# Kernel optimization log

Hardware: AMD Instinct MI355X
Metric: run time of the kernel (lower is better)

The kernel has to match this reference:

```python
import jax, jax.numpy as jnp
import numpy as np

N = 50000        # n_nodes
E = 640000       # n_edges
D = 128          # d_model (in_dim == out_dim)
H = 8            # num_heads
DH = D // H      # head dim = 16
EPS = 1e-5


def _batchnorm(x, g, b):
    # BatchNorm1d, training-mode batch statistics (biased variance)
    mu = jnp.mean(x, axis=0)
    var = jnp.mean((x - mu) ** 2, axis=0)
    return (x - mu) * jax.lax.rsqrt(var + EPS) * g + b


def setup_inputs() -> dict:
    key = jax.random.key(0)
    ks = jax.random.split(key, 16)
    s = 0.05
    h = jax.random.normal(ks[0], (N, D), jnp.float32)
    src = jax.random.randint(ks[1], (E,), 0, N)
    # guarantee every node has >= 1 incoming edge (avoids z == 0)
    dst = jnp.concatenate([jnp.arange(N), jax.random.randint(ks[2], (E - N,), 0, N)])
    return {
        "h": h,
        "src": src,
        "dst": dst,
        "WQ": jax.random.normal(ks[3], (D, D), jnp.float32) * s,
        "WK": jax.random.normal(ks[4], (D, D), jnp.float32) * s,
        "WV": jax.random.normal(ks[5], (D, D), jnp.float32) * s,
        "WO": jax.random.normal(ks[6], (D, D), jnp.float32) * s,
        "bO": jnp.zeros((D,), jnp.float32),
        "W1": jax.random.normal(ks[7], (2 * D, D), jnp.float32) * s,
        "b1": jnp.zeros((2 * D,), jnp.float32),
        "W2": jax.random.normal(ks[8], (D, 2 * D), jnp.float32) * s,
        "b2": jnp.zeros((D,), jnp.float32),
        "bn1_g": jnp.ones((D,), jnp.float32),
        "bn1_b": jnp.zeros((D,), jnp.float32),
        "bn2_g": jnp.ones((D,), jnp.float32),
        "bn2_b": jnp.zeros((D,), jnp.float32),
    }


def reference(h, src, dst, WQ, WK, WV, WO, bO, W1, b1, W2, b2, bn1_g, bn1_b, bn2_g, bn2_b):
    n = h.shape[0]
    # projections -> [N, H, DH]
    Q = (h @ WQ.T).reshape(n, H, DH)
    K = (h @ WK.T).reshape(n, H, DH)
    V = (h @ WV.T).reshape(n, H, DH)
    # per-edge score: sum(K[src] * Q[dst]) -> [E, H]; clamp/exp (scaled_exp)
    score = jnp.sum(K[src] * Q[dst], axis=-1) / np.sqrt(DH)
    score = jnp.exp(jnp.clip(score, -5.0, 5.0))
    # scatter-sum weighted values and normalizers to destination nodes
    wV = jax.ops.segment_sum(V[src] * score[..., None], dst, num_segments=n)  # [N,H,DH]
    z = jax.ops.segment_sum(score, dst, num_segments=n)                       # [N,H]
    attn = (wV / z[..., None]).reshape(n, D)
    # O projection + residual + BN1
    h1 = _batchnorm(h + (attn @ WO.T + bO), bn1_g, bn1_b)
    # FFN + residual + BN2
    f = jax.nn.relu(h1 @ W1.T + b1) @ W2.T + b2
    return _batchnorm(h1 + f, bn2_g, bn2_b)
```

## Files before the change

### kernel.cpp

```cpp
#include <hip/hip_runtime.h>
#include <math.h>


#define ND128 16384
typedef _Float16 f16;
typedef __attribute__((ext_vector_type(8))) _Float16 h8;
typedef __attribute__((ext_vector_type(4))) _Float16 h4;
typedef __attribute__((ext_vector_type(2))) _Float16 h2;
typedef __attribute__((ext_vector_type(4))) float f4;

__device__ __forceinline__ float fdot2h(h2 a, h2 b) {
#if __has_builtin(__builtin_amdgcn_fdot2)
    return __builtin_amdgcn_fdot2(a, b, 0.f, false);
#else
    return (float)a[0] * (float)b[0] + (float)a[1] * (float)b[1];
#endif
}

__device__ __forceinline__ float fast_exp2(float x) {
#if __has_builtin(__builtin_amdgcn_exp2f)
    return __builtin_amdgcn_exp2f(x);
#else
    return exp2f(x);
#endif
}

template <int CTRL>
__device__ __forceinline__ float dppadd(float x) {
    int t = __builtin_amdgcn_update_dpp(0, __float_as_int(x), CTRL, 0xF, 0xF, false);
    return x + __int_as_float(t);
}
__device__ __forceinline__ float wsum8(float p) {
    p = dppadd<0xB1>(p);
    p = dppadd<0x4E>(p);
    p = dppadd<0x141>(p);
    return p;
}

__global__ __launch_bounds__(256) void k_prep_hist(
    const float* __restrict__ h, f16* __restrict__ hb,
    const float* __restrict__ WQ, const float* __restrict__ WK,
    const float* __restrict__ WV, const float* __restrict__ WO,
    const float* __restrict__ W2,
    f16* __restrict__ Wqb, f16* __restrict__ Wkb,
    f16* __restrict__ Wvb, f16* __restrict__ Wob, f16* __restrict__ W2b,
    int* __restrict__ cursor, const int* __restrict__ dst,
    int N, int E, int nhb)
{
    const int tid = threadIdx.x;
    if (blockIdx.x < (unsigned)nhb) {
        int e = blockIdx.x * 256 + tid;
        if (e < E) atomicAdd(&cursor[dst[e]], 1);
        return;
    }
    const int p = blockIdx.x - nhb;
    const int slab = p >> 1, my = p & 1;
#pragma unroll
    for (int it2 = 0; it2 < 4; ++it2) {
        int it = my * 4 + it2;
        int cid = it * 256 + tid;
        int lane = cid & 63;
        int m = (cid >> 6) & 7;
        int kb = cid >> 9;
        int row = slab * 128 + m * 16 + (lane & 15);
        int col = kb * 32 + (lane >> 4) * 8;
        f16 o8[8];
        if (row < N) {
            const float* pp = h + (size_t)row * 128 + col;
            float4 f0 = *(const float4*)pp;
            float4 f1 = *(const float4*)(pp + 4);
            o8[0] = (f16)f0.x; o8[1] = (f16)f0.y; o8[2] = (f16)f0.z; o8[3] = (f16)f0.w;
            o8[4] = (f16)f1.x; o8[5] = (f16)f1.y; o8[6] = (f16)f1.z; o8[7] = (f16)f1.w;
        } else {
#pragma unroll
            for (int j = 0; j < 8; ++j) o8[j] = (f16)0.f;
        }
        *(h8*)(hb + (size_t)slab * ND128 + (size_t)cid * 8) = *(const h8*)o8;
    }
    if (slab < 6 && my == 1) {
        const float* Wsrc; f16* dstw; int K, base;
        if (slab < 4) {
            Wsrc = slab == 0 ? WQ : slab == 1 ? WK : slab == 2 ? WV : WO;
            dstw = slab == 0 ? Wqb : slab == 1 ? Wkb : slab == 2 ? Wvb : Wob;
            K = 128; base = 0;
        } else {
            Wsrc = W2; dstw = W2b; K = 256; base = (slab - 4) * 2048;
        }
#pragma unroll
        for (int it = 0; it < 8; ++it) {
            int cid = base + it * 256 + tid;
            int lane = cid & 63;
            int kb, nt;
            if (K == 128) { kb = (cid >> 6) & 3; nt = cid >> 8; }
            else          { kb = (cid >> 6) & 7; nt = cid >> 9; }
            int row = nt * 16 + (lane & 15);
            int col = kb * 32 + (lane >> 4) * 8;
            const float* pp = Wsrc + (size_t)row * K + col;
            f16 o8[8];
#pragma unroll
            for (int j = 0; j < 8; ++j) o8[j] = (f16)pp[j];
            *(h8*)(dstw + (size_t)cid * 8) = *(const h8*)o8;
        }
    }
}

__global__ __launch_bounds__(256) void k_qkv_scan(
    const f16* __restrict__ hb, const f16* __restrict__ Wqb,
    const f16* __restrict__ Wkb, const f16* __restrict__ Wvb,
    f16* __restrict__ Qb, f16* __restrict__ KVb,
    int* __restrict__ cursor, int* __restrict__ rowptr,
    int* __restrict__ ready, int N, int nsb)
{
    const int tid = threadIdx.x;
    if (blockIdx.x < (unsigned)nsb) {
        const int b = blockIdx.x;
        int base = b * 2048 + tid * 8;
        int loc[8];
        int s = 0;
#pragma unroll
        for (int j = 0; j < 8; ++j) {
            int idx = base + j;
            loc[j] = (idx < N) ? cursor[idx] : 0;
            s += loc[j];
        }
        __shared__ int part[256];
        part[tid] = s;
        __syncthreads();
        for (int off = 1; off < 256; off <<= 1) {
            int v = (tid >= off) ? part[tid - off] : 0;
            __syncthreads();
            part[tid] += v;
            __syncthreads();
        }
        __shared__ int sboff_sh;
        if (tid == 0) {
            int prev = 0;
            if (b > 0) {
                int r;
                while ((r = __hip_atomic_load(&ready[b - 1], __ATOMIC_ACQUIRE,
                                              __HIP_MEMORY_SCOPE_AGENT)) == 0) {}
                prev = r - 1;
            }
            int btotal = part[255];
            __hip_atomic_store(&ready[b], prev + btotal + 1, __ATOMIC_RELEASE,
                               __HIP_MEMORY_SCOPE_AGENT);
            sboff_sh = prev;
            if (b == nsb - 1) rowptr[N] = prev + btotal;
        }
        __syncthreads();
        int run = sboff_sh + (tid ? part[tid - 1] : 0);
#pragma unroll
        for (int j = 0; j < 8; ++j) {
            int idx = base + j;
            if (idx < N) { rowptr[idx] = run; cursor[idx] = run; run += loc[j]; }
        }
        return;
    }
    const int b2 = blockIdx.x - nsb;
    const int slab = b2 / 6, r6 = b2 % 6;
    const int oidx = r6 >> 1, mh = r6 & 1;
    const int w = tid >> 6, lane = tid & 63;
    const f16* __restrict__ Wb = oidx == 0 ? Wqb : oidx == 1 ? Wkb : Wvb;
    const f16* A = hb + (size_t)slab * ND128;

    h8 bfr[2][4];
#pragma unroll
    for (int nt = 0; nt < 2; ++nt)
#pragma unroll
        for (int kb = 0; kb < 4; ++kb)
            bfr[nt][kb] = *(const h8*)(Wb + (size_t)(((2 * w + nt) * 4 + kb) * 64 + lane) * 8);

    f4 acc[4][2];
    f4 zero = {0.f, 0.f, 0.f, 0.f};
#pragma unroll
    for (int m = 0; m < 4; ++m) { acc[m][0] = zero; acc[m][1] = zero; }

#pragma unroll
    for (int m = 0; m < 4; ++m) {
        int mg = mh * 4 + m;
#pragma unroll
        for (int kb = 0; kb < 4; ++kb) {
            h8 a = *(const h8*)(A + (size_t)((kb * 8 + mg) * 64 + lane) * 8);
            acc[m][0] = __builtin_amdgcn_mfma_f32_16x16x32_f16(bfr[0][kb], a, acc[m][0], 0, 0, 0);
            acc[m][1] = __builtin_amdgcn_mfma_f32_16x16x32_f16(bfr[1][kb], a, acc[m][1], 0, 0, 0);
        }
    }

    const int rl = lane & 15, quad = lane >> 4;
#pragma unroll
    for (int m = 0; m < 4; ++m) {
        int gr = slab * 128 + (mh * 4 + m) * 16 + rl;
        if (gr < N) {
#pragma unroll
            for (int nt = 0; nt < 2; ++nt) {
                h4 o;
                o[0] = (f16)acc[m][nt][0]; o[1] = (f16)acc[m][nt][1];
                o[2] = (f16)acc[m][nt][2]; o[3] = (f16)acc[m][nt][3];
                int col = w * 32 + nt * 16 + quad * 4;
                if (oidx == 0) {
                    *(h4*)(Qb + (size_t)gr * 128 + col) = o;
                } else {
                    *(h4*)(KVb + (size_t)gr * 256 + (oidx == 1 ? col : 128 + col)) = o;
                }
            }
        }
    }
}

__global__ __launch_bounds__(256) void k_scatter(
    const int* __restrict__ src, const int* __restrict__ dst,
    int* __restrict__ cursor, int* __restrict__ csr_src, int E)
{
    int e = blockIdx.x * 256 + threadIdx.x;
    if (e < E) {
        int pos = atomicAdd(&cursor[dst[e]], 1);
        csr_src[pos] = src[e];
    }
}

__global__ __launch_bounds__(256) void k_attn(
    const f16* __restrict__ Qb, const f16* __restrict__ KVb,
    const int* __restrict__ rowptr, const int* __restrict__ csr_src,
    f16* __restrict__ attnf, int N)
{
    const int node = blockIdx.x * 4 + (threadIdx.x >> 6);
    const int lane = threadIdx.x & 63;
    if (node >= N) return;
    const int beg = rowptr[node], end = rowptr[node + 1];

    h2 qs;
    {
        h2 q2 = ((const h2*)(Qb + (size_t)node * 128))[lane];
        const float SCL = 0.25f * 1.44269504f;
        qs[0] = (f16)((float)q2[0] * SCL);
        qs[1] = (f16)((float)q2[1] * SCL);
    }
    const float CLP = 5.f * 1.44269504f;

    const h2* __restrict__ KV2 = (const h2*)KVb;

    h2 accA, accB;
    accA[0] = (f16)0.f; accA[1] = (f16)0.f;
    accB[0] = (f16)0.f; accB[1] = (f16)0.f;
    float z = 0.f;

    int i = beg;
    for (; i + 7 < end; i += 8) {
        int s[8];
#pragma unroll
        for (int u = 0; u < 8; ++u) s[u] = csr_src[i + u];
        h2 kk[8], vv[8];
#pragma unroll
        for (int u = 0; u < 8; ++u) {
            const h2* row = KV2 + (size_t)s[u] * 128;
            kk[u] = row[lane];
            vv[u] = row[64 + lane];
        }
        float sc[8];
#pragma unroll
        for (int u = 0; u < 8; ++u) {
            float p = wsum8(fdot2h(qs, kk[u]));
            sc[u] = fast_exp2(fminf(fmaxf(p, -CLP), CLP));
        }
#pragma unroll
        for (int u = 0; u < 8; ++u) z += sc[u];
#pragma unroll
        for (int u = 0; u < 8; ++u) {
            h2 c; c[0] = (f16)sc[u]; c[1] = (f16)sc[u];
            if (u & 1) accB += c * vv[u]; else accA += c * vv[u];
        }
    }
    if (i + 3 < end) {
        int s[4];
#pragma unroll
        for (int u = 0; u < 4; ++u) s[u] = csr_src[i + u];
        h2 kk[4], vv[4];
#pragma unroll
        for (int u = 0; u < 4; ++u) {
            const h2* row = KV2 + (size_t)s[u] * 128;
            kk[u] = row[lane];
            vv[u] = row[64 + lane];
        }
#pragma unroll
        for (int u = 0; u < 4; ++u) {
            float p = wsum8(fdot2h(qs, kk[u]));
            float scu = fast_exp2(fminf(fmaxf(p, -CLP), CLP));
            z += scu;
            h2 c; c[0] = (f16)scu; c[1] = (f16)scu;
            if (u & 1) accB += c * vv[u]; else accA += c * vv[u];
        }
        i += 4;
    }
    for (; i < end; ++i) {
        int s0 = csr_src[i];
        const h2* row = KV2 + (size_t)s0 * 128;
        h2 k0 = row[lane];
        h2 v0 = row[64 + lane];
        float p0 = wsum8(fdot2h(qs, k0));
        float sc0 = fast_exp2(fminf(fmaxf(p0, -CLP), CLP));
        z += sc0;
        h2 c0; c0[0] = (f16)sc0; c0[1] = (f16)sc0;
        accA += c0 * v0;
    }

    float inv = 1.f / z;
    float ax = ((float)accA[0] + (float)accB[0]) * inv;
    float ay = ((float)accA[1] + (float)accB[1]) * inv;
    h2 o2;
    o2[0] = (f16)ax; o2[1] = (f16)ay;
    int slab = node >> 7, m = (node >> 4) & 7, lr = node & 15;
    int kb = lane >> 4, quad2 = (lane & 15) >> 2, j = (lane & 3) * 2;
    *(h2*)(attnf + (size_t)slab * ND128 +
           (size_t)(((kb * 8 + m) * 64 + lr + 16 * quad2) * 8 + j)) = o2;
}

__global__ __launch_bounds__(256) void k_oproj(
    const f16* __restrict__ attnf, const f16* __restrict__ Wob,
    const float* __restrict__ h, const float* __restrict__ bO,
    f16* __restrict__ t1b, float* __restrict__ bn, int N)
{
    __shared__ float csum[128], csq[128];
    const int tid = threadIdx.x, slab = blockIdx.x, mh = blockIdx.y;
    const int w = tid >> 6, lane = tid & 63;
    if (tid < 128) { csum[tid] = 0.f; csq[tid] = 0.f; }
    __syncthreads();
    const f16* A = attnf + (size_t)slab * ND128;

    h8 bfr[2][4];
#pragma unroll
    for (int nt = 0; nt < 2; ++nt)
#pragma unroll
        for (int kb = 0; kb < 4; ++kb)
            bfr[nt][kb] = *(const h8*)(Wob + (size_t)(((2 * w + nt) * 4 + kb) * 64 + lane) * 8);

    f4 acc[4][2];
    f4 zero = {0.f, 0.f, 0.f, 0.f};
#pragma unroll
    for (int m = 0; m < 4; ++m) { acc[m][0] = zero; acc[m][1] = zero; }
#pragma unroll
    for (int m = 0; m < 4; ++m) {
        int mg = mh * 4 + m;
#pragma unroll
        for (int kb = 0; kb < 4; ++kb) {
            h8 a = *(const h8*)(A + (size_t)((kb * 8 + mg) * 64 + lane) * 8);
            acc[m][0] = __builtin_amdgcn_mfma_f32_16x16x32_f16(bfr[0][kb], a, acc[m][0], 0, 0, 0);
            acc[m][1] = __builtin_amdgcn_mfma_f32_16x16x32_f16(bfr[1][kb], a, acc[m][1], 0, 0, 0);
        }
    }

    const int rl = lane & 15, quad = lane >> 4;
    float4 bo[2];
#pragma unroll
    for (int nt = 0; nt < 2; ++nt)
        bo[nt] = *(const float4*)(bO + w * 32 + nt * 16 + quad * 4);
    float pcs[2][4], pcq[2][4];
#pragma unroll
    for (int nt = 0; nt < 2; ++nt)
#pragma unroll
        for (int r = 0; r < 4; ++r) { pcs[nt][r] = 0.f; pcq[nt][r] = 0.f; }

#pragma unroll
    for (int m = 0; m < 4; ++m) {
        int mg = mh * 4 + m;
        int gr = slab * 128 + mg * 16 + rl;
        if (gr < N) {
#pragma unroll
            for (int nt = 0; nt < 2; ++nt) {
                int col0 = w * 32 + nt * 16 + quad * 4;
                float4 hv = *(const float4*)(h + (size_t)gr * 128 + col0);
                float v0 = acc[m][nt][0] + hv.x + bo[nt].x;
                float v1 = acc[m][nt][1] + hv.y + bo[nt].y;
                float v2 = acc[m][nt][2] + hv.z + bo[nt].z;
                float v3 = acc[m][nt][3] + hv.w + bo[nt].w;
                h4 o; o[0] = (f16)v0; o[1] = (f16)v1; o[2] = (f16)v2; o[3] = (f16)v3;
                *(h4*)(t1b + (size_t)slab * ND128 +
                       (size_t)(((w * 8 + mg) * 64 + (nt * 2 + (quad >> 1)) * 16 + rl) * 8 +
                                (quad & 1) * 4)) = o;
                pcs[nt][0] += v0; pcq[nt][0] += v0 * v0;
                pcs[nt][1] += v1; pcq[nt][1] += v1 * v1;
                pcs[nt][2] += v2; pcq[nt][2] += v2 * v2;
                pcs[nt][3] += v3; pcq[nt][3] += v3 * v3;
            }
        }
    }
#pragma unroll
    for (int nt = 0; nt < 2; ++nt)
#pragma unroll
        for (int r = 0; r < 4; ++r) {
            float s = pcs[nt][r], q = pcq[nt][r];
            s += __shfl_xor(s, 8, 16); q += __shfl_xor(q, 8, 16);
            s += __shfl_xor(s, 4, 16); q += __shfl_xor(q, 4, 16);
            s += __shfl_xor(s, 2, 16); q += __shfl_xor(q, 2, 16);
            s += __shfl_xor(s, 1, 16); q += __shfl_xor(q, 1, 16);
            if (rl == 0) {
                int cl = w * 32 + nt * 16 + quad * 4 + r;
                atomicAdd(&csum[cl], s);
                atomicAdd(&csq[cl], q);
            }
        }
    __syncthreads();
    if (tid < 128) {
        atomicAdd(bn + tid, csum[tid]);
        atomicAdd(bn + 128 + tid, csq[tid]);
    }
}

__global__ __launch_bounds__(128) void k_fold1(
    const float* __restrict__ bn, const float* __restrict__ g1,
    const float* __restrict__ bb1, const float* __restrict__ W1,
    const float* __restrict__ b1, f16* __restrict__ W1b,
    float* __restrict__ badj, float* __restrict__ sfold,
    float* __restrict__ bfold, int N)
{
    const int o = blockIdx.x, i = threadIdx.x;
    float invN = 1.f / (float)N;
    float mu = bn[i] * invN;
    float var = bn[128 + i] * invN - mu * mu;
    float s = g1[i] * rsqrtf(var + 1e-5f);
    float bb = bb1[i] - mu * s;
    if (o == 0) { sfold[i] = s; bfold[i] = bb; }
    float wv = W1[(size_t)o * 128 + i];
    __shared__ float red[128];
    red[i] = wv * bb;
    const int nt = o >> 4, lanelow = o & 15;
    const int kb = i >> 5, quad = (i >> 3) & 3, j = i & 7;
    W1b[(size_t)(((nt * 4 + kb) * 64 + lanelow + 16 * quad) * 8 + j)] = (f16)(wv * s);
    __syncthreads();
#pragma unroll
    for (int off = 64; off; off >>= 1) {
        if (i < off) red[i] += red[i + off];
        __syncthreads();
    }
    if (i == 0) badj[o] = b1[o] + red[0];
}

__global__ __launch_bounds__(256) void k_ffn1(
    const f16* __restrict__ t1b, const f16* __restrict__ W1b,
    const float* __restrict__ badj, f16* __restrict__ ub, int N)
{
    const int slab = blockIdx.x, ch = blockIdx.y, mh = blockIdx.z;
    const int w = threadIdx.x >> 6, lane = threadIdx.x & 63;
    const f16* A = t1b + (size_t)slab * ND128;

    h8 bfr[2][4];
#pragma unroll
    for (int nt = 0; nt < 2; ++nt)
#pragma unroll
        for (int kb = 0; kb < 4; ++kb) {
            int ntg = ch * 8 + 2 * w + nt;
            bfr[nt][kb] = *(const h8*)(W1b + (size_t)((ntg * 4 + kb) * 64 + lane) * 8);
        }

    f4 acc[4][2];
    f4 zero = {0.f, 0.f, 0.f, 0.f};
#pragma unroll
    for (int m = 0; m < 4; ++m) { acc[m][0] = zero; acc[m][1] = zero; }
#pragma unroll
    for (int m = 0; m < 4; ++m) {
        int mg = mh * 4 + m;
#pragma unroll
        for (int kb = 0; kb < 4; ++kb) {
            h8 a = *(const h8*)(A + (size_t)((kb * 8 + mg) * 64 + lane) * 8);
            acc[m][0] = __builtin_amdgcn_mfma_f32_16x16x32_f16(bfr[0][kb], a, acc[m][0], 0, 0, 0);
            acc[m][1] = __builtin_amdgcn_mfma_f32_16x16x32_f16(bfr[1][kb], a, acc[m][1], 0, 0, 0);
        }
    }

    const int rl = lane & 15, quad = lane >> 4;
    const int kbu = ch * 4 + w;
    float4 ba[2];
#pragma unroll
    for (int nt = 0; nt < 2; ++nt)
        ba[nt] = *(const float4*)(badj + ch * 128 + w * 32 + nt * 16 + quad * 4);
#pragma unroll
    for (int m = 0; m < 4; ++m) {
        int mg = mh * 4 + m;
        int gr = slab * 128 + mg * 16 + rl;
        if (gr < N) {
#pragma unroll
            for (int nt = 0; nt < 2; ++nt) {
                h4 o;
                o[0] = (f16)fmaxf(acc[m][nt][0] + ba[nt].x, 0.f);
                o[1] = (f16)fmaxf(acc[m][nt][1] + ba[nt].y, 0.f);
                o[2] = (f16)fmaxf(acc[m][nt][2] + ba[nt].z, 0.f);
                o[3] = (f16)fmaxf(acc[m][nt][3] + ba[nt].w, 0.f);
                *(h4*)(ub + (size_t)slab * 32768 +
                       (size_t)(((kbu * 8 + mg) * 64 + (nt * 2 + (quad >> 1)) * 16 + rl) * 8 +
                                (quad & 1) * 4)) = o;
            }
        }
    }
}

__global__ __launch_bounds__(256) void k_ffn2(
    const f16* __restrict__ ub, const f16* __restrict__ W2b,
    const f16* __restrict__ t1b,
    const float* __restrict__ sfold, const float* __restrict__ bfold,
    const float* __restrict__ b2, float* __restrict__ out,
    float* __restrict__ bn, int N)
{
    __shared__ float csum[128], csq[128], sS[128], sB[128];
    const int tid = threadIdx.x, slab = blockIdx.x, mh = blockIdx.y;
    const int w = tid >> 6, lane = tid & 63;
    if (tid < 128) {
        csum[tid] = 0.f; csq[tid] = 0.f;
        sS[tid] = sfold[tid]; sB[tid] = bfold[tid] + b2[tid];
    }
    __syncthreads();
    const f16* A = ub + (size_t)slab * 32768;
    const f16* T1 = t1b + (size_t)slab * ND128;

    h8 bfr[2][8];
#pragma unroll
    for (int nt = 0; nt < 2; ++nt)
#pragma unroll
        for (int kb = 0; kb < 8; ++kb)
            bfr[nt][kb] = *(const h8*)(W2b + (size_t)(((2 * w + nt) * 8 + kb) * 64 + lane) * 8);

    f4 acc[4][2];
    f4 zero = {0.f, 0.f, 0.f, 0.f};
#pragma unroll
    for (int m = 0; m < 4; ++m) { acc[m][0] = zero; acc[m][1] = zero; }
#pragma unroll
    for (int m = 0; m < 4; ++m) {
        int mg = mh * 4 + m;
#pragma unroll
        for (int kb = 0; kb < 8; ++kb) {
            h8 a = *(const h8*)(A + (size_t)((kb * 8 + mg) * 64 + lane) * 8);
            acc[m][0] = __builtin_amdgcn_mfma_f32_16x16x32_f16(bfr[0][kb], a, acc[m][0], 0, 0, 0);
            acc[m][1] = __builtin_amdgcn_mfma_f32_16x16x32_f16(bfr[1][kb], a, acc[m][1], 0, 0, 0);
        }
    }

    const int rl = lane & 15, quad = lane >> 4;
    float pcs[2][4], pcq[2][4];
#pragma unroll
    for (int nt = 0; nt < 2; ++nt)
#pragma unroll
        for (int r = 0; r < 4; ++r) { pcs[nt][r] = 0.f; pcq[nt][r] = 0.f; }

#pragma unroll
    for (int m = 0; m < 4; ++m) {
        int mg = mh * 4 + m;
        int gr = slab * 128 + mg * 16 + rl;
        if (gr < N) {
#pragma unroll
            for (int nt = 0; nt < 2; ++nt) {
                int col0 = w * 32 + nt * 16 + quad * 4;
                h4 t1v = *(const h4*)(T1 +
                    (size_t)(((w * 8 + mg) * 64 + (nt * 2 + (quad >> 1)) * 16 + rl) * 8 +
                             (quad & 1) * 4));
                float4 ss = *(const float4*)&sS[col0];
                float4 sb = *(const float4*)&sB[col0];
                float4 o;
                o.x = acc[m][nt][0] + fmaf(ss.x, (float)t1v[0], sb.x);
                o.y = acc[m][nt][1] + fmaf(ss.y, (float)t1v[1], sb.y);
                o.z = acc[m][nt][2] + fmaf(ss.z, (float)t1v[2], sb.z);
                o.w = acc[m][nt][3] + fmaf(ss.w, (float)t1v[3], sb.w);
                *(float4*)(out + (size_t)gr * 128 + col0) = o;
                pcs[nt][0] += o.x; pcq[nt][0] += o.x * o.x;
                pcs[nt][1] += o.y; pcq[nt][1] += o.y * o.y;
                pcs[nt][2] += o.z; pcq[nt][2] += o.z * o.z;
                pcs[nt][3] += o.w; pcq[nt][3] += o.w * o.w;
            }
        }
    }
#pragma unroll
    for (int nt = 0; nt < 2; ++nt)
#pragma unroll
        for (int r = 0; r < 4; ++r) {
            float s = pcs[nt][r], q = pcq[nt][r];
            s += __shfl_xor(s, 8, 16); q += __shfl_xor(q, 8, 16);
            s += __shfl_xor(s, 4, 16); q += __shfl_xor(q, 4, 16);
            s += __shfl_xor(s, 2, 16); q += __shfl_xor(q, 2, 16);
            s += __shfl_xor(s, 1, 16); q += __shfl_xor(q, 1, 16);
            if (rl == 0) {
                int cl = w * 32 + nt * 16 + quad * 4 + r;
                atomicAdd(&csum[cl], s);
                atomicAdd(&csq[cl], q);
            }
        }
    __syncthreads();
    if (tid < 128) {
        atomicAdd(bn + 256 + tid, csum[tid]);
        atomicAdd(bn + 384 + tid, csq[tid]);
    }
}

__global__ __launch_bounds__(256) void k_bn2(
    float* __restrict__ out, const float* __restrict__ bn,
    const float* __restrict__ g2, const float* __restrict__ bb2, int N)
{
    __shared__ float sS[128], sB[128];
    const int tid = threadIdx.x;
    if (tid < 128) {
        float invN = 1.f / (float)N;
        float mu = bn[256 + tid] * invN;
        float var = bn[384 + tid] * invN - mu * mu;
        float scl = g2[tid] * rsqrtf(var + 1e-5f);
        sS[tid] = scl;
        sB[tid] = bb2[tid] - mu * scl;
    }
    __syncthreads();
    size_t idx = (size_t)blockIdx.x * 256 + tid;
    size_t total = (size_t)N * 32;
    if (idx < total) {
        int c0 = (int)((idx * 4) & 127);
        float4 v = *(const float4*)(out + idx * 4);
        v.x = fmaf(v.x, sS[c0 + 0], sB[c0 + 0]);
        v.y = fmaf(v.y, sS[c0 + 1], sB[c0 + 1]);
        v.z = fmaf(v.z, sS[c0 + 2], sB[c0 + 2]);
        v.w = fmaf(v.w, sS[c0 + 3], sB[c0 + 3]);
        *(float4*)(out + idx * 4) = v;
    }
}

extern "C" void kernel_launch(void* const* d_in, const int* in_sizes, int n_in,
                              void* d_out, int out_size, void* d_ws, size_t ws_size,
                              hipStream_t stream)
{
    const float* h   = (const float*)d_in[0];
    const int*   src = (const int*)d_in[1];
    const int*   dst = (const int*)d_in[2];
    const float* WQ  = (const float*)d_in[3];
    const float* WK  = (const float*)d_in[4];
    const float* WV  = (const float*)d_in[5];
    const float* WO  = (const float*)d_in[6];
    const float* bO  = (const float*)d_in[7];
    const float* W1  = (const float*)d_in[8];
    const float* b1  = (const float*)d_in[9];
    const float* W2  = (const float*)d_in[10];
    const float* b2  = (const float*)d_in[11];
    const float* g1  = (const float*)d_in[12];
    const float* bb1 = (const float*)d_in[13];
    const float* g2  = (const float*)d_in[14];
    const float* bb2 = (const float*)d_in[15];
    float* out = (float*)d_out;

    int N = in_sizes[0] / 128;
    int E = in_sizes[1];
    const int slabs = (N + 127) / 128;
    const int nsb = (N + 2047) / 2048;
    const int nhb = (E + 255) / 256;
    const size_t B1 = (size_t)slabs * 32768;

    char* Wp = (char*)d_ws;
    f16* hb  = (f16*)Wp;
    f16* Qb  = (f16*)(Wp + B1);
    f16* KVb = (f16*)(Wp + 2 * B1);
    f16* ub  = (f16*)(Wp + B1);
    f16* t1b = (f16*)(Wp + 3 * B1);
    const size_t base = 4 * B1;
    f16* Wqb = (f16*)(Wp + base);
    f16* Wkb = (f16*)(Wp + base + 32768);
    f16* Wvb = (f16*)(Wp + base + 65536);
    f16* Wob = (f16*)(Wp + base + 98304);
    f16* W1b = (f16*)(Wp + base + 131072);
    f16* W2b = (f16*)(Wp + base + 196608);
    float* badj  = (float*)(Wp + base + 262144);
    float* sfold = (float*)(Wp + base + 263168);
    float* bfold = (float*)(Wp + base + 263680);
    float* bn    = (float*)(Wp + base + 264192);
    int* ready   = (int*)(Wp + base + 266240);
    int* cursor  = (int*)(Wp + base + 266496);
    int* rowptr  = (int*)(Wp + base + 266496 + (size_t)N * 4);
    int* csr     = (int*)(Wp + base + 266496 + (size_t)N * 8 + 8);

    hipMemsetAsync(Wp + base + 264192, 0, 2304 + (size_t)N * 4, stream);
    k_prep_hist<<<nhb + slabs * 2, 256, 0, stream>>>(
        h, hb, WQ, WK, WV, WO, W2, Wqb, Wkb, Wvb, Wob, W2b, cursor, dst, N, E, nhb);
    k_qkv_scan<<<nsb + slabs * 6, 256, 0, stream>>>(
        hb, Wqb, Wkb, Wvb, Qb, KVb, cursor, rowptr, ready, N, nsb);
    k_scatter<<<nhb, 256, 0, stream>>>(src, dst, cursor, csr, E);
    k_attn<<<(N + 3) / 4, 256, 0, stream>>>(Qb, KVb, rowptr, csr, hb, N);
    k_oproj<<<dim3(slabs, 2), 256, 0, stream>>>(hb, Wob, h, bO, t1b, bn, N);
    k_fold1<<<256, 128, 0, stream>>>(bn, g1, bb1, W1, b1, W1b, badj, sfold, bfold, N);
    k_ffn1<<<dim3(slabs, 2, 2), 256, 0, stream>>>(t1b, W1b, badj, ub, N);
    k_ffn2<<<dim3(slabs, 2), 256, 0, stream>>>(ub, W2b, t1b, sfold, bfold, b2, out, bn, N);
    k_bn2<<<(int)(((size_t)N * 32 + 255) / 256), 256, 0, stream>>>(out, bn, g2, bb2, N);
}
```

Baseline: 340.1 us.

## Fuse front and back stages into persistent cooperative kernels with grid syncs

Merges the memset, fp16 conversion, histogram, QKV projection and prefix scan into one cooperative kernel, and merges O-projection, BN1 fold, FFN1, FFN2 and the BN2 apply into another. Stages are separated by grid.sync, and each block loops over work units with a grid stride. The chained decoupled scan is replaced by a two-pass block-sum scan. This removes several kernel launches and the memset, at the cost of grid-wide barriers, a grid sized to occupancy, and less parallelism in stages that had many blocks.

```diff
diff --git a/kernel.cpp b/kernel.cpp
--- a/kernel.cpp
+++ b/kernel.cpp
@@ -1,5 +1,8 @@
 #include <hip/hip_runtime.h>
+#include <hip/hip_cooperative_groups.h>
 #include <math.h>
+
+namespace cg = cooperative_groups;
 
 
 #define ND128 16384
@@ -37,81 +40,156 @@
     return p;
 }
 
-__global__ __launch_bounds__(256) void k_prep_hist(
+__global__ __launch_bounds__(256) void k_front(
     const float* __restrict__ h, f16* __restrict__ hb,
     const float* __restrict__ WQ, const float* __restrict__ WK,
     const float* __restrict__ WV, const float* __restrict__ WO,
     const float* __restrict__ W2,
     f16* __restrict__ Wqb, f16* __restrict__ Wkb,
     f16* __restrict__ Wvb, f16* __restrict__ Wob, f16* __restrict__ W2b,
-    int* __restrict__ cursor, const int* __restrict__ dst,
-    int N, int E, int nhb)
-{
-    const int tid = threadIdx.x;
-    if (blockIdx.x < (unsigned)nhb) {
-        int e = blockIdx.x * 256 + tid;
-        if (e < E) atomicAdd(&cursor[dst[e]], 1);
-        return;
-    }
-    const int p = blockIdx.x - nhb;
-    const int slab = p >> 1, my = p & 1;
-#pragma unroll
-    for (int it2 = 0; it2 < 4; ++it2) {
-        int it = my * 4 + it2;
-        int cid = it * 256 + tid;
-        int lane = cid & 63;
-        int m = (cid >> 6) & 7;
-        int kb = cid >> 9;
-        int row = slab * 128 + m * 16 + (lane & 15);
-        int col = kb * 32 + (lane >> 4) * 8;
-        f16 o8[8];
-        if (row < N) {
-            const float* pp = h + (size_t)row * 128 + col;
-            float4 f0 = *(const float4*)pp;
-            float4 f1 = *(const float4*)(pp + 4);
-            o8[0] = (f16)f0.x; o8[1] = (f16)f0.y; o8[2] = (f16)f0.z; o8[3] = (f16)f0.w;
-            o8[4] = (f16)f1.x; o8[5] = (f16)f1.y; o8[6] = (f16)f1.z; o8[7] = (f16)f1.w;
-        } else {
-#pragma unroll
-            for (int j = 0; j < 8; ++j) o8[j] = (f16)0.f;
-        }
-        *(h8*)(hb + (size_t)slab * ND128 + (size_t)cid * 8) = *(const h8*)o8;
-    }
-    if (slab < 6 && my == 1) {
-        const float* Wsrc; f16* dstw; int K, base;
-        if (slab < 4) {
-            Wsrc = slab == 0 ? WQ : slab == 1 ? WK : slab == 2 ? WV : WO;
-            dstw = slab == 0 ? Wqb : slab == 1 ? Wkb : slab == 2 ? Wvb : Wob;
-            K = 128; base = 0;
-        } else {
-            Wsrc = W2; dstw = W2b; K = 256; base = (slab - 4) * 2048;
-        }
-#pragma unroll
-        for (int it = 0; it < 8; ++it) {
-            int cid = base + it * 256 + tid;
-            int lane = cid & 63;
-            int kb, nt;
-            if (K == 128) { kb = (cid >> 6) & 3; nt = cid >> 8; }
-            else          { kb = (cid >> 6) & 7; nt = cid >> 9; }
-            int row = nt * 16 + (lane & 15);
-            int col = kb * 32 + (lane >> 4) * 8;
-            const float* pp = Wsrc + (size_t)row * K + col;
-            f16 o8[8];
-#pragma unroll
-            for (int j = 0; j < 8; ++j) o8[j] = (f16)pp[j];
-            *(h8*)(dstw + (size_t)cid * 8) = *(const h8*)o8;
-        }
-    }
-}
-
-__global__ __launch_bounds__(256) void k_qkv_scan(
-    const f16* __restrict__ hb, const f16* __restrict__ Wqb,
-    const f16* __restrict__ Wkb, const f16* __restrict__ Wvb,
     f16* __restrict__ Qb, f16* __restrict__ KVb,
     int* __restrict__ cursor, int* __restrict__ rowptr,
-    int* __restrict__ ready, int N, int nsb)
+    int* __restrict__ bsum, float* __restrict__ bn,
+    const int* __restrict__ dst, int N, int E, int nhb, int nsb, int slabs)
 {
+    cg::grid_group grid = cg::this_grid();
     const int tid = threadIdx.x;
+    const int G = gridDim.x;
+    __shared__ int part[256];
+    __shared__ int sboff_sh;
+
+    for (int idx = blockIdx.x * 256 + tid; idx < N; idx += G * 256) cursor[idx] = 0;
+    if (blockIdx.x == 0) { bn[tid] = 0.f; bn[tid + 256] = 0.f; }
+    const int U0 = slabs * 2 + 6;
+    for (int u = blockIdx.x; u < U0; u += G) {
+        if (u < slabs * 2) {
+            const int slab = u >> 1, my = u & 1;
+#pragma unroll
+            for (int it2 = 0; it2 < 4; ++it2) {
+                int it = my * 4 + it2;
+                int cid = it * 256 + tid;
+                int lane = cid & 63;
+                int m = (cid >> 6) & 7;
+                int kb = cid >> 9;
+                int row = slab * 128 + m * 16 + (lane & 15);
+                int col = kb * 32 + (lane >> 4) * 8;
+                f16 o8[8];
+                if (row < N) {
+                    const float* pp = h + (size_t)row * 128 + col;
+                    float4 f0 = *(const float4*)pp;
+                    float4 f1 = *(const float4*)(pp + 4);
+                    o8[0] = (f16)f0.x; o8[1] = (f16)f0.y; o8[2] = (f16)f0.z; o8[3] = (f16)f0.w;
+                    o8[4] = (f16)f1.x; o8[5] = (f16)f1.y; o8[6] = (f16)f1.z; o8[7] = (f16)f1.w;
+                } else {
+#pragma unroll
+                    for (int j = 0; j < 8; ++j) o8[j] = (f16)0.f;
+                }
+                *(h8*)(hb + (size_t)slab * ND128 + (size_t)cid * 8) = *(const h8*)o8;
+            }
+        } else {
+            const int ws = u - slabs * 2;
+            const float* Wsrc; f16* dstw; int K, base;
+            if (ws < 4) {
+                Wsrc = ws == 0 ? WQ : ws == 1 ? WK : ws == 2 ? WV : WO;
+                dstw = ws == 0 ? Wqb : ws == 1 ? Wkb : ws == 2 ? Wvb : Wob;
+                K = 128; base = 0;
+            } else {
+                Wsrc = W2; dstw = W2b; K = 256; base = (ws - 4) * 2048;
+            }
+#pragma unroll
+            for (int it = 0; it < 8; ++it) {
+                int cid = base + it * 256 + tid;
+                int lane = cid & 63;
+                int kb, nt;
+                if (K == 128) { kb = (cid >> 6) & 3; nt = cid >> 8; }
+                else          { kb = (cid >> 6) & 7; nt = cid >> 9; }
+                int row = nt * 16 + (lane & 15);
+                int col = kb * 32 + (lane >> 4) * 8;
+                const float* pp = Wsrc + (size_t)row * K + col;
+                f16 o8[8];
+#pragma unroll
+                for (int j = 0; j < 8; ++j) o8[j] = (f16)pp[j];
+                *(h8*)(dstw + (size_t)cid * 8) = *(const h8*)o8;
+            }
+        }
+    }
+    grid.sync();
+
+    const int U1 = nhb + slabs * 6;
+    for (int u = blockIdx.x; u < U1; u += G) {
+        if (u < nhb) {
+            int e = u * 256 + tid;
+            if (e < E) atomicAdd(&cursor[dst[e]], 1);
+        } else {
+            const int b2 = u - nhb;
+            const int slab = b2 / 6, r6 = b2 % 6;
+            const int oidx = r6 >> 1, mh = r6 & 1;
+            const int w = tid >> 6, lane = tid & 63;
+            const f16* __restrict__ Wb = oidx == 0 ? Wqb : oidx == 1 ? Wkb : Wvb;
+            const f16* A = hb + (size_t)slab * ND128;
+
+            h8 bfr[2][4];
+#pragma unroll
+            for (int nt = 0; nt < 2; ++nt)
+#pragma unroll
+                for (int kb = 0; kb < 4; ++kb)
+                    bfr[nt][kb] = *(const h8*)(Wb + (size_t)(((2 * w + nt) * 4 + kb) * 64 + lane) * 8);
+
+            f4 acc[4][2];
+            f4 zero = {0.f, 0.f, 0.f, 0.f};
+#pragma unroll
+            for (int m = 0; m < 4; ++m) { acc[m][0] = zero; acc[m][1] = zero; }
+#pragma unroll
+            for (int m = 0; m < 4; ++m) {
+                int mg = mh * 4 + m;
+#pragma unroll
+                for (int kb = 0; kb < 4; ++kb) {
+                    h8 a = *(const h8*)(A + (size_t)((kb * 8 + mg) * 64 + lane) * 8);
+                    acc[m][0] = __builtin_amdgcn_mfma_f32_16x16x32_f16(bfr[0][kb], a, acc[m][0], 0, 0, 0);
+                    acc[m][1] = __builtin_amdgcn_mfma_f32_16x16x32_f16(bfr[1][kb], a, acc[m][1], 0, 0, 0);
+                }
+            }
+            const int rl = lane & 15, quad = lane >> 4;
+#pragma unroll
+            for (int m = 0; m < 4; ++m) {
+                int gr = slab * 128 + (mh * 4 + m) * 16 + rl;
+                if (gr < N) {
+#pragma unroll
+                    for (int nt = 0; nt < 2; ++nt) {
+                        h4 o;
+                        o[0] = (f16)acc[m][nt][0]; o[1] = (f16)acc[m][nt][1];
+                        o[2] = (f16)acc[m][nt][2]; o[3] = (f16)acc[m][nt][3];
+                        int col = w * 32 + nt * 16 + quad * 4;
+                        if (oidx == 0) {
+                            *(h4*)(Qb + (size_t)gr * 128 + col) = o;
+                        } else {
+                            *(h4*)(KVb + (size_t)gr * 256 + (oidx == 1 ? col : 128 + col)) = o;
+                        }
+                    }
+                }
+            }
+        }
+    }
+    grid.sync();
+
+    if (blockIdx.x < (unsigned)nsb) {
+        int base = blockIdx.x * 2048 + tid * 8;
+        int s = 0;
+#pragma unroll
+        for (int j = 0; j < 8; ++j) {
+            int idx = base + j;
+            if (idx < N) s += cursor[idx];
+        }
+        part[tid] = s;
+        __syncthreads();
+        for (int off = 128; off; off >>= 1) {
+            if (tid < off) part[tid] += part[tid + off];
+            __syncthreads();
+        }
+        if (tid == 0) bsum[blockIdx.x] = part[0];
+    }
+    grid.sync();
+
     if (blockIdx.x < (unsigned)nsb) {
         const int b = blockIdx.x;
         int base = b * 2048 + tid * 8;
@@ -123,7 +201,6 @@
             loc[j] = (idx < N) ? cursor[idx] : 0;
             s += loc[j];
         }
-        __shared__ int part[256];
         part[tid] = s;
         __syncthreads();
         for (int off = 1; off < 256; off <<= 1) {
@@ -132,20 +209,11 @@
             part[tid] += v;
             __syncthreads();
         }
-        __shared__ int sboff_sh;
         if (tid == 0) {
             int prev = 0;
-            if (b > 0) {
-                int r;
-                while ((r = __hip_atomic_load(&ready[b - 1], __ATOMIC_ACQUIRE,
-                                              __HIP_MEMORY_SCOPE_AGENT)) == 0) {}
-                prev = r - 1;
-            }
-            int btotal = part[255];
-            __hip_atomic_store(&ready[b], prev + btotal + 1, __ATOMIC_RELEASE,
-                               __HIP_MEMORY_SCOPE_AGENT);
+            for (int i2 = 0; i2 < b; ++i2) prev += bsum[i2];
             sboff_sh = prev;
-            if (b == nsb - 1) rowptr[N] = prev + btotal;
+            if (b == nsb - 1) rowptr[N] = prev + part[255];
         }
         __syncthreads();
         int run = sboff_sh + (tid ? part[tid - 1] : 0);
@@ -153,56 +221,6 @@
         for (int j = 0; j < 8; ++j) {
             int idx = base + j;
             if (idx < N) { rowptr[idx] = run; cursor[idx] = run; run += loc[j]; }
-        }
-        return;
-    }
-    const int b2 = blockIdx.x - nsb;
-    const int slab = b2 / 6, r6 = b2 % 6;
-    const int oidx = r6 >> 1, mh = r6 & 1;
-    const int w = tid >> 6, lane = tid & 63;
-    const f16* __restrict__ Wb = oidx == 0 ? Wqb : oidx == 1 ? Wkb : Wvb;
-    const f16* A = hb + (size_t)slab * ND128;
-
-    h8 bfr[2][4];
-#pragma unroll
-    for (int nt = 0; nt < 2; ++nt)
-#pragma unroll
-        for (int kb = 0; kb < 4; ++kb)
-            bfr[nt][kb] = *(const h8*)(Wb + (size_t)(((2 * w + nt) * 4 + kb) * 64 + lane) * 8);
-
-    f4 acc[4][2];
-    f4 zero = {0.f, 0.f, 0.f, 0.f};
-#pragma unroll
-    for (int m = 0; m < 4; ++m) { acc[m][0] = zero; acc[m][1] = zero; }
-
-#pragma unroll
-    for (int m = 0; m < 4; ++m) {
-        int mg = mh * 4 + m;
-#pragma unroll
-        for (int kb = 0; kb < 4; ++kb) {
-            h8 a = *(const h8*)(A + (size_t)((kb * 8 + mg) * 64 + lane) * 8);
-            acc[m][0] = __builtin_amdgcn_mfma_f32_16x16x32_f16(bfr[0][kb], a, acc[m][0], 0, 0, 0);
-            acc[m][1] = __builtin_amdgcn_mfma_f32_16x16x32_f16(bfr[1][kb], a, acc[m][1], 0, 0, 0);
-        }
-    }
-
-    const int rl = lane & 15, quad = lane >> 4;
-#pragma unroll
-    for (int m = 0; m < 4; ++m) {
-        int gr = slab * 128 + (mh * 4 + m) * 16 + rl;
-        if (gr < N) {
-#pragma unroll
-            for (int nt = 0; nt < 2; ++nt) {
-                h4 o;
-                o[0] = (f16)acc[m][nt][0]; o[1] = (f16)acc[m][nt][1];
-                o[2] = (f16)acc[m][nt][2]; o[3] = (f16)acc[m][nt][3];
-                int col = w * 32 + nt * 16 + quad * 4;
-                if (oidx == 0) {
-                    *(h4*)(Qb + (size_t)gr * 128 + col) = o;
-                } else {
-                    *(h4*)(KVb + (size_t)gr * 256 + (oidx == 1 ? col : 128 + col)) = o;
-                }
-            }
         }
     }
 }
@@ -314,285 +332,278 @@
            (size_t)(((kb * 8 + m) * 64 + lr + 16 * quad2) * 8 + j)) = o2;
 }
 
-__global__ __launch_bounds__(256) void k_oproj(
+__global__ __launch_bounds__(256) void k_back(
     const f16* __restrict__ attnf, const f16* __restrict__ Wob,
     const float* __restrict__ h, const float* __restrict__ bO,
-    f16* __restrict__ t1b, float* __restrict__ bn, int N)
+    f16* __restrict__ t1b, float* __restrict__ bn,
+    const float* __restrict__ g1, const float* __restrict__ bb1,
+    const float* __restrict__ W1, const float* __restrict__ b1,
+    f16* __restrict__ W1b, float* __restrict__ badj,
+    float* __restrict__ sfold, float* __restrict__ bfold,
+    f16* __restrict__ ub, const f16* __restrict__ W2b,
+    const float* __restrict__ b2, float* __restrict__ out,
+    const float* __restrict__ g2, const float* __restrict__ bb2,
+    int N, int slabs)
 {
-    __shared__ float csum[128], csq[128];
-    const int tid = threadIdx.x, slab = blockIdx.x, mh = blockIdx.y;
+    cg::grid_group grid = cg::this_grid();
+    const int tid = threadIdx.x;
+    const int G = gridDim.x;
     const int w = tid >> 6, lane = tid & 63;
-    if (tid < 128) { csum[tid] = 0.f; csq[tid] = 0.f; }
-    __syncthreads();
-    const f16* A = attnf + (size_t)slab * ND128;
-
-    h8 bfr[2][4];
-#pragma unroll
-    for (int nt = 0; nt < 2; ++nt)
-#pragma unroll
-        for (int kb = 0; kb < 4; ++kb)
-            bfr[nt][kb] = *(const h8*)(Wob + (size_t)(((2 * w + nt) * 4 + kb) * 64 + lane) * 8);
-
-    f4 acc[4][2];
-    f4 zero = {0.f, 0.f, 0.f, 0.f};
-#pragma unroll
-    for (int m = 0; m < 4; ++m) { acc[m][0] = zero; acc[m][1] = zero; }
-#pragma unroll
-    for (int m = 0; m < 4; ++m) {
-        int mg = mh * 4 + m;
-#pragma unroll
-        for (int kb = 0; kb < 4; ++kb) {
-            h8 a = *(const h8*)(A + (size_t)((kb * 8 + mg) * 64 + lane) * 8);
-            acc[m][0] = __builtin_amdgcn_mfma_f32_16x16x32_f16(bfr[0][kb], a, acc[m][0], 0, 0, 0);
-            acc[m][1] = __builtin_amdgcn_mfma_f32_16x16x32_f16(bfr[1][kb], a, acc[m][1], 0, 0, 0);
-        }
-    }
-
     const int rl = lane & 15, quad = lane >> 4;
-    float4 bo[2];
-#pragma unroll
-    for (int nt = 0; nt < 2; ++nt)
-        bo[nt] = *(const float4*)(bO + w * 32 + nt * 16 + quad * 4);
-    float pcs[2][4], pcq[2][4];
-#pragma unroll
-    for (int nt = 0; nt < 2; ++nt)
-#pragma unroll
-        for (int r = 0; r < 4; ++r) { pcs[nt][r] = 0.f; pcq[nt][r] = 0.f; }
-
-#pragma unroll
-    for (int m = 0; m < 4; ++m) {
-        int mg = mh * 4 + m;
-        int gr = slab * 128 + mg * 16 + rl;
-        if (gr < N) {
-#pragma unroll
-            for (int nt = 0; nt < 2; ++nt) {
-                int col0 = w * 32 + nt * 16 + quad * 4;
-                float4 hv = *(const float4*)(h + (size_t)gr * 128 + col0);
-                float v0 = acc[m][nt][0] + hv.x + bo[nt].x;
-                float v1 = acc[m][nt][1] + hv.y + bo[nt].y;
-                float v2 = acc[m][nt][2] + hv.z + bo[nt].z;
-                float v3 = acc[m][nt][3] + hv.w + bo[nt].w;
-                h4 o; o[0] = (f16)v0; o[1] = (f16)v1; o[2] = (f16)v2; o[3] = (f16)v3;
-                *(h4*)(t1b + (size_t)slab * ND128 +
-                       (size_t)(((w * 8 + mg) * 64 + (nt * 2 + (quad >> 1)) * 16 + rl) * 8 +
-                                (quad & 1) * 4)) = o;
-                pcs[nt][0] += v0; pcq[nt][0] += v0 * v0;
-                pcs[nt][1] += v1; pcq[nt][1] += v1 * v1;
-                pcs[nt][2] += v2; pcq[nt][2] += v2 * v2;
-                pcs[nt][3] += v3; pcq[nt][3] += v3 * v3;
-            }
-        }
-    }
-#pragma unroll
-    for (int nt = 0; nt < 2; ++nt)
-#pragma unroll
-        for (int r = 0; r < 4; ++r) {
-            float s = pcs[nt][r], q = pcq[nt][r];
-            s += __shfl_xor(s, 8, 16); q += __shfl_xor(q, 8, 16);
-            s += __shfl_xor(s, 4, 16); q += __shfl_xor(q, 4, 16);
-            s += __shfl_xor(s, 2, 16); q += __shfl_xor(q, 2, 16);
-            s += __shfl_xor(s, 1, 16); q += __shfl_xor(q, 1, 16);
-            if (rl == 0) {
-                int cl = w * 32 + nt * 16 + quad * 4 + r;
-                atomicAdd(&csum[cl], s);
-                atomicAdd(&csq[cl], q);
-            }
-        }
-    __syncthreads();
-    if (tid < 128) {
-        atomicAdd(bn + tid, csum[tid]);
-        atomicAdd(bn + 128 + tid, csq[tid]);
-    }
-}
-
-__global__ __launch_bounds__(128) void k_fold1(
-    const float* __restrict__ bn, const float* __restrict__ g1,
-    const float* __restrict__ bb1, const float* __restrict__ W1,
-    const float* __restrict__ b1, f16* __restrict__ W1b,
-    float* __restrict__ badj, float* __restrict__ sfold,
-    float* __restrict__ bfold, int N)
-{
-    const int o = blockIdx.x, i = threadIdx.x;
-    float invN = 1.f / (float)N;
-    float mu = bn[i] * invN;
-    float var = bn[128 + i] * invN - mu * mu;
-    float s = g1[i] * rsqrtf(var + 1e-5f);
-    float bb = bb1[i] - mu * s;
-    if (o == 0) { sfold[i] = s; bfold[i] = bb; }
-    float wv = W1[(size_t)o * 128 + i];
+    __shared__ float csum[128], csq[128], sS[128], sB[128];
     __shared__ float red[128];
-    red[i] = wv * bb;
-    const int nt = o >> 4, lanelow = o & 15;
-    const int kb = i >> 5, quad = (i >> 3) & 3, j = i & 7;
-    W1b[(size_t)(((nt * 4 + kb) * 64 + lanelow + 16 * quad) * 8 + j)] = (f16)(wv * s);
-    __syncthreads();
-#pragma unroll
-    for (int off = 64; off; off >>= 1) {
-        if (i < off) red[i] += red[i + off];
+
+    {
+        h8 bfr[2][4];
+#pragma unroll
+        for (int nt = 0; nt < 2; ++nt)
+#pragma unroll
+            for (int kb = 0; kb < 4; ++kb)
+                bfr[nt][kb] = *(const h8*)(Wob + (size_t)(((2 * w + nt) * 4 + kb) * 64 + lane) * 8);
+        float4 bo[2];
+#pragma unroll
+        for (int nt = 0; nt < 2; ++nt)
+            bo[nt] = *(const float4*)(bO + w * 32 + nt * 16 + quad * 4);
+
+        for (int u = blockIdx.x; u < slabs * 2; u += G) {
+            const int slab = u >> 1, mh = u & 1;
+            if (tid < 128) { csum[tid] = 0.f; csq[tid] = 0.f; }
+            __syncthreads();
+            const f16* A = attnf + (size_t)slab * ND128;
+
+            f4 acc[4][2];
+            f4 zero = {0.f, 0.f, 0.f, 0.f};
+#pragma unroll
+            for (int m = 0; m < 4; ++m) { acc[m][0] = zero; acc[m][1] = zero; }
+#pragma unroll
+            for (int m = 0; m < 4; ++m) {
+                int mg = mh * 4 + m;
+#pragma unroll
+                for (int kb = 0; kb < 4; ++kb) {
+                    h8 a = *(const h8*)(A + (size_t)((kb * 8 + mg) * 64 + lane) * 8);
+                    acc[m][0] = __builtin_amdgcn_mfma_f32_16x16x32_f16(bfr[0][kb], a, acc[m][0], 0, 0, 0);
+                    acc[m][1] = __builtin_amdgcn_mfma_f32_16x16x32_f16(bfr[1][kb], a, acc[m][1], 0, 0, 0);
+                }
+            }
+            float pcs[2][4], pcq[2][4];
+#pragma unroll
+            for (int nt = 0; nt < 2; ++nt)
+#pragma unroll
+                for (int r = 0; r < 4; ++r) { pcs[nt][r] = 0.f; pcq[nt][r] = 0.f; }
+#pragma unroll
+            for (int m = 0; m < 4; ++m) {
+                int mg = mh * 4 + m;
+                int gr = slab * 128 + mg * 16 + rl;
+                if (gr < N) {
+#pragma unroll
+                    for (int nt = 0; nt < 2; ++nt) {
+                        int col0 = w * 32 + nt * 16 + quad * 4;
+                        float4 hv = *(const float4*)(h + (size_t)gr * 128 + col0);
+                        float v0 = acc[m][nt][0] + hv.x + bo[nt].x;
+                        float v1 = acc[m][nt][1] + hv.y + bo[nt].y;
+                        float v2 = acc[m][nt][2] + hv.z + bo[nt].z;
+                        float v3 = acc[m][nt][3] + hv.w + bo[nt].w;
+                        h4 o; o[0] = (f16)v0; o[1] = (f16)v1; o[2] = (f16)v2; o[3] = (f16)v3;
+                        *(h4*)(t1b + (size_t)slab * ND128 +
+                               (size_t)(((w * 8 + mg) * 64 + (nt * 2 + (quad >> 1)) * 16 + rl) * 8 +
+                                        (quad & 1) * 4)) = o;
+                        pcs[nt][0] += v0; pcq[nt][0] += v0 * v0;
+                        pcs[nt][1] += v1; pcq[nt][1] += v1 * v1;
+                        pcs[nt][2] += v2; pcq[nt][2] += v2 * v2;
+                        pcs[nt][3] += v3; pcq[nt][3] += v3 * v3;
+                    }
+                }
+            }
+#pragma unroll
+            for (int nt = 0; nt < 2; ++nt)
+#pragma unroll
+                for (int r = 0; r < 4; ++r) {
+                    float s = pcs[nt][r], q = pcq[nt][r];
+                    s += __shfl_xor(s, 8, 16); q += __shfl_xor(q, 8, 16);
+                    s += __shfl_xor(s, 4, 16); q += __shfl_xor(q, 4, 16);
+                    s += __shfl_xor(s, 2, 16); q += __shfl_xor(q, 2, 16);
+                    s += __shfl_xor(s, 1, 16); q += __shfl_xor(q, 1, 16);
+                    if (rl == 0) {
+                        int cl = w * 32 + nt * 16 + quad * 4 + r;
+                        atomicAdd(&csum[cl], s);
+                        atomicAdd(&csq[cl], q);
+                    }
+                }
+            __syncthreads();
+            if (tid < 128) {
+                atomicAdd(bn + tid, csum[tid]);
+                atomicAdd(bn + 128 + tid, csq[tid]);
+            }
+            __syncthreads();
+        }
+    }
+    grid.sync();
+
+    for (int u = blockIdx.x; u < 256; u += G) {
+        const int o = u, i = tid & 127;
+        if (tid < 128) {
+            float invN = 1.f / (float)N;
+            float mu = bn[i] * invN;
+            float var = bn[128 + i] * invN - mu * mu;
+            float s = g1[i] * rsqrtf(var + 1e-5f);
+            float bb = bb1[i] - mu * s;
+            if (o == 0) { sfold[i] = s; bfold[i] = bb; }
+            float wv = W1[(size_t)o * 128 + i];
+            red[i] = wv * bb;
+            const int nt = o >> 4, lanelow = o & 15;
+            const int kb = i >> 5, qq = (i >> 3) & 3, j = i & 7;
+            W1b[(size_t)(((nt * 4 + kb) * 64 + lanelow + 16 * qq) * 8 + j)] = (f16)(wv * s);
+        }
         __syncthreads();
-    }
-    if (i == 0) badj[o] = b1[o] + red[0];
-}
-
-__global__ __launch_bounds__(256) void k_ffn1(
-    const f16* __restrict__ t1b, const f16* __restrict__ W1b,
-    const float* __restrict__ badj, f16* __restrict__ ub, int N)
-{
-    const int slab = blockIdx.x, ch = blockIdx.y, mh = blockIdx.z;
-    const int w = threadIdx.x >> 6, lane = threadIdx.x & 63;
-    const f16* A = t1b + (size_t)slab * ND128;
-
-    h8 bfr[2][4];
-#pragma unroll
-    for (int nt = 0; nt < 2; ++nt)
-#pragma unroll
-        for (int kb = 0; kb < 4; ++kb) {
-            int ntg = ch * 8 + 2 * w + nt;
-            bfr[nt][kb] = *(const h8*)(W1b + (size_t)((ntg * 4 + kb) * 64 + lane) * 8);
-        }
-
-    f4 acc[4][2];
-    f4 zero = {0.f, 0.f, 0.f, 0.f};
-#pragma unroll
-    for (int m = 0; m < 4; ++m) { acc[m][0] = zero; acc[m][1] = zero; }
-#pragma unroll
-    for (int m = 0; m < 4; ++m) {
-        int mg = mh * 4 + m;
-#pragma unroll
-        for (int kb = 0; kb < 4; ++kb) {
-            h8 a = *(const h8*)(A + (size_t)((kb * 8 + mg) * 64 + lane) * 8);
-            acc[m][0] = __builtin_amdgcn_mfma_f32_16x16x32_f16(bfr[0][kb], a, acc[m][0], 0, 0, 0);
-            acc[m][1] = __builtin_amdgcn_mfma_f32_16x16x32_f16(bfr[1][kb], a, acc[m][1], 0, 0, 0);
-        }
-    }
-
-    const int rl = lane & 15, quad = lane >> 4;
-    const int kbu = ch * 4 + w;
-    float4 ba[2];
-#pragma unroll
-    for (int nt = 0; nt < 2; ++nt)
-        ba[nt] = *(const float4*)(badj + ch * 128 + w * 32 + nt * 16 + quad * 4);
-#pragma unroll
-    for (int m = 0; m < 4; ++m) {
-        int mg = mh * 4 + m;
-        int gr = slab * 128 + mg * 16 + rl;
-        if (gr < N) {
-#pragma unroll
-            for (int nt = 0; nt < 2; ++nt) {
-                h4 o;
-                o[0] = (f16)fmaxf(acc[m][nt][0] + ba[nt].x, 0.f);
-                o[1] = (f16)fmaxf(acc[m][nt][1] + ba[nt].y, 0.f);
-                o[2] = (f16)fmaxf(acc[m][nt][2] + ba[nt].z, 0.f);
-                o[3] = (f16)fmaxf(acc[m][nt][3] + ba[nt].w, 0.f);
-                *(h4*)(ub + (size_t)slab * 32768 +
-                       (size_t)(((kbu * 8 + mg) * 64 + (nt * 2 + (quad >> 1)) * 16 + rl) * 8 +
-                                (quad & 1) * 4)) = o;
-            }
-        }
-    }
-}
-
-__global__ __launch_bounds__(256) void k_ffn2(
-    const f16* __restrict__ ub, const f16* __restrict__ W2b,
-    const f16* __restrict__ t1b,
-    const float* __restrict__ sfold, const float* __restrict__ bfold,
-    const float* __restrict__ b2, float* __restrict__ out,
-    float* __restrict__ bn, int N)
-{
-    __shared__ float csum[128], csq[128], sS[128], sB[128];
-    const int tid = threadIdx.x, slab = blockIdx.x, mh = blockIdx.y;
-    const int w = tid >> 6, lane = tid & 63;
-    if (tid < 128) {
-        csum[tid] = 0.f; csq[tid] = 0.f;
-        sS[tid] = sfold[tid]; sB[tid] = bfold[tid] + b2[tid];
-    }
-    __syncthreads();
-    const f16* A = ub + (size_t)slab * 32768;
-    const f16* T1 = t1b + (size_t)slab * ND128;
-
-    h8 bfr[2][8];
-#pragma unroll
-    for (int nt = 0; nt < 2; ++nt)
-#pragma unroll
-        for (int kb = 0; kb < 8; ++kb)
-            bfr[nt][kb] = *(const h8*)(W2b + (size_t)(((2 * w + nt) * 8 + kb) * 64 + lane) * 8);
-
-    f4 acc[4][2];
-    f4 zero = {0.f, 0.f, 0.f, 0.f};
-#pragma unroll
-    for (int m = 0; m < 4; ++m) { acc[m][0] = zero; acc[m][1] = zero; }
-#pragma unroll
-    for (int m = 0; m < 4; ++m) {
-        int mg = mh * 4 + m;
-#pragma unroll
-        for (int kb = 0; kb < 8; ++kb) {
-            h8 a = *(const h8*)(A + (size_t)((kb * 8 + mg) * 64 + lane) * 8);
-            acc[m][0] = __builtin_amdgcn_mfma_f32_16x16x32_f16(bfr[0][kb], a, acc[m][0], 0, 0, 0);
-            acc[m][1] = __builtin_amdgcn_mfma_f32_16x16x32_f16(bfr[1][kb], a, acc[m][1], 0, 0, 0);
-        }
-    }
-
-    const int rl = lane & 15, quad = lane >> 4;
-    float pcs[2][4], pcq[2][4];
-#pragma unroll
-    for (int nt = 0; nt < 2; ++nt)
-#pragma unroll
-        for (int r = 0; r < 4; ++r) { pcs[nt][r] = 0.f; pcq[nt][r] = 0.f; }
-
-#pragma unroll
-    for (int m = 0; m < 4; ++m) {
-        int mg = mh * 4 + m;
-        int gr = slab * 128 + mg * 16 + rl;
-        if (gr < N) {
-#pragma unroll
-            for (int nt = 0; nt < 2; ++nt) {
-                int col0 = w * 32 + nt * 16 + quad * 4;
-                h4 t1v = *(const h4*)(T1 +
-                    (size_t)(((w * 8 + mg) * 64 + (nt * 2 + (quad >> 1)) * 16 + rl) * 8 +
-                             (quad & 1) * 4));
-                float4 ss = *(const float4*)&sS[col0];
-                float4 sb = *(const float4*)&sB[col0];
-                float4 o;
-                o.x = acc[m][nt][0] + fmaf(ss.x, (float)t1v[0], sb.x);
-                o.y = acc[m][nt][1] + fmaf(ss.y, (float)t1v[1], sb.y);
-                o.z = acc[m][nt][2] + fmaf(ss.z, (float)t1v[2], sb.z);
-                o.w = acc[m][nt][3] + fmaf(ss.w, (float)t1v[3], sb.w);
-                *(float4*)(out + (size_t)gr * 128 + col0) = o;
-                pcs[nt][0] += o.x; pcq[nt][0] += o.x * o.x;
-                pcs[nt][1] += o.y; pcq[nt][1] += o.y * o.y;
-                pcs[nt][2] += o.z; pcq[nt][2] += o.z * o.z;
-                pcs[nt][3] += o.w; pcq[nt][3] += o.w * o.w;
-            }
-        }
-    }
-#pragma unroll
-    for (int nt = 0; nt < 2; ++nt)
-#pragma unroll
-        for (int r = 0; r < 4; ++r) {
-            float s = pcs[nt][r], q = pcq[nt][r];
-            s += __shfl_xor(s, 8, 16); q += __shfl_xor(q, 8, 16);
-            s += __shfl_xor(s, 4, 16); q += __shfl_xor(q, 4, 16);
-            s += __shfl_xor(s, 2, 16); q += __shfl_xor(q, 2, 16);
-            s += __shfl_xor(s, 1, 16); q += __shfl_xor(q, 1, 16);
-            if (rl == 0) {
-                int cl = w * 32 + nt * 16 + quad * 4 + r;
-                atomicAdd(&csum[cl], s);
-                atomicAdd(&csq[cl], q);
-            }
-        }
-    __syncthreads();
-    if (tid < 128) {
-        atomicAdd(bn + 256 + tid, csum[tid]);
-        atomicAdd(bn + 384 + tid, csq[tid]);
-    }
-}
-
-__global__ __launch_bounds__(256) void k_bn2(
-    float* __restrict__ out, const float* __restrict__ bn,
-    const float* __restrict__ g2, const float* __restrict__ bb2, int N)
-{
-    __shared__ float sS[128], sB[128];
-    const int tid = threadIdx.x;
+        for (int off = 64; off; off >>= 1) {
+            if (tid < off) red[tid] += red[tid + off];
+            __syncthreads();
+        }
+        if (tid == 0) badj[o] = b1[o] + red[0];
+        __syncthreads();
+    }
+    grid.sync();
+
+    for (int u = blockIdx.x; u < slabs * 4; u += G) {
+        const int slab = u >> 2, ch = (u >> 1) & 1, mh = u & 1;
+        const f16* A = t1b + (size_t)slab * ND128;
+
+        h8 bfr[2][4];
+#pragma unroll
+        for (int nt = 0; nt < 2; ++nt)
+#pragma unroll
+            for (int kb = 0; kb < 4; ++kb) {
+                int ntg = ch * 8 + 2 * w + nt;
+                bfr[nt][kb] = *(const h8*)(W1b + (size_t)((ntg * 4 + kb) * 64 + lane) * 8);
+            }
+
+        f4 acc[4][2];
+        f4 zero = {0.f, 0.f, 0.f, 0.f};
+#pragma unroll
+        for (int m = 0; m < 4; ++m) { acc[m][0] = zero; acc[m][1] = zero; }
+#pragma unroll
+        for (int m = 0; m < 4; ++m) {
+            int mg = mh * 4 + m;
+#pragma unroll
+            for (int kb = 0; kb < 4; ++kb) {
+                h8 a = *(const h8*)(A + (size_t)((kb * 8 + mg) * 64 + lane) * 8);
+                acc[m][0] = __builtin_amdgcn_mfma_f32_16x16x32_f16(bfr[0][kb], a, acc[m][0], 0, 0, 0);
+                acc[m][1] = __builtin_amdgcn_mfma_f32_16x16x32_f16(bfr[1][kb], a, acc[m][1], 0, 0, 0);
+            }
+        }
+        const int kbu = ch * 4 + w;
+        float4 ba[2];
+#pragma unroll
+        for (int nt = 0; nt < 2; ++nt)
+            ba[nt] = *(const float4*)(badj + ch * 128 + w * 32 + nt * 16 + quad * 4);
+#pragma unroll
+        for (int m = 0; m < 4; ++m) {
+            int mg = mh * 4 + m;
+            int gr = slab * 128 + mg * 16 + rl;
+            if (gr < N) {
+#pragma unroll
+                for (int nt = 0; nt < 2; ++nt) {
+                    h4 o;
+                    o[0] = (f16)fmaxf(acc[m][nt][0] + ba[nt].x, 0.f);
+                    o[1] = (f16)fmaxf(acc[m][nt][1] + ba[nt].y, 0.f);
+                    o[2] = (f16)fmaxf(acc[m][nt][2] + ba[nt].z, 0.f);
+                    o[3] = (f16)fmaxf(acc[m][nt][3] + ba[nt].w, 0.f);
+                    *(h4*)(ub + (size_t)slab * 32768 +
+                           (size_t)(((kbu * 8 + mg) * 64 + (nt * 2 + (quad >> 1)) * 16 + rl) * 8 +
+                                    (quad & 1) * 4)) = o;
+                }
+            }
+        }
+    }
+    grid.sync();
+
+    {
+        h8 bfr[2][8];
+#pragma unroll
+        for (int nt = 0; nt < 2; ++nt)
+#pragma unroll
+            for (int kb = 0; kb < 8; ++kb)
+                bfr[nt][kb] = *(const h8*)(W2b + (size_t)(((2 * w + nt) * 8 + kb) * 64 + lane) * 8);
+        if (tid < 128) { sS[tid] = sfold[tid]; sB[tid] = bfold[tid] + b2[tid]; }
+        __syncthreads();
+
+        for (int u = blockIdx.x; u < slabs * 2; u += G) {
+            const int slab = u >> 1, mh = u & 1;
+            if (tid < 128) { csum[tid] = 0.f; csq[tid] = 0.f; }
+            __syncthreads();
+            const f16* A = ub + (size_t)slab * 32768;
+            const f16* T1 = t1b + (size_t)slab * ND128;
+
+            f4 acc[4][2];
+            f4 zero = {0.f, 0.f, 0.f, 0.f};
+#pragma unroll
+            for (int m = 0; m < 4; ++m) { acc[m][0] = zero; acc[m][1] = zero; }
+#pragma unroll
+            for (int m = 0; m < 4; ++m) {
+                int mg = mh * 4 + m;
+#pragma unroll
+                for (int kb = 0; kb < 8; ++kb) {
+                    h8 a = *(const h8*)(A + (size_t)((kb * 8 + mg) * 64 + lane) * 8);
+                    acc[m][0] = __builtin_amdgcn_mfma_f32_16x16x32_f16(bfr[0][kb], a, acc[m][0], 0, 0, 0);
+                    acc[m][1] = __builtin_amdgcn_mfma_f32_16x16x32_f16(bfr[1][kb], a, acc[m][1], 0, 0, 0);
+                }
+            }
+            float pcs[2][4], pcq[2][4];
+#pragma unroll
+            for (int nt = 0; nt < 2; ++nt)
+#pragma unroll
+                for (int r = 0; r < 4; ++r) { pcs[nt][r] = 0.f; pcq[nt][r] = 0.f; }
+#pragma unroll
+            for (int m = 0; m < 4; ++m) {
+                int mg = mh * 4 + m;
+                int gr = slab * 128 + mg * 16 + rl;
+                if (gr < N) {
+#pragma unroll
+                    for (int nt = 0; nt < 2; ++nt) {
+                        int col0 = w * 32 + nt * 16 + quad * 4;
+                        h4 t1v = *(const h4*)(T1 +
+                            (size_t)(((w * 8 + mg) * 64 + (nt * 2 + (quad >> 1)) * 16 + rl) * 8 +
+                                     (quad & 1) * 4));
+                        float4 ss = *(const float4*)&sS[col0];
+                        float4 sb = *(const float4*)&sB[col0];
+                        float4 o;
+                        o.x = acc[m][nt][0] + fmaf(ss.x, (float)t1v[0], sb.x);
+                        o.y = acc[m][nt][1] + fmaf(ss.y, (float)t1v[1], sb.y);
+                        o.z = acc[m][nt][2] + fmaf(ss.z, (float)t1v[2], sb.z);
+                        o.w = acc[m][nt][3] + fmaf(ss.w, (float)t1v[3], sb.w);
+                        *(float4*)(out + (size_t)gr * 128 + col0) = o;
+                        pcs[nt][0] += o.x; pcq[nt][0] += o.x * o.x;
+                        pcs[nt][1] += o.y; pcq[nt][1] += o.y * o.y;
+                        pcs[nt][2] += o.z; pcq[nt][2] += o.z * o.z;
+                        pcs[nt][3] += o.w; pcq[nt][3] += o.w * o.w;
+                    }
+                }
+            }
+#pragma unroll
+            for (int nt = 0; nt < 2; ++nt)
+#pragma unroll
+                for (int r = 0; r < 4; ++r) {
+                    float s = pcs[nt][r], q = pcq[nt][r];
+                    s += __shfl_xor(s, 8, 16); q += __shfl_xor(q, 8, 16);
+                    s += __shfl_xor(s, 4, 16); q += __shfl_xor(q, 4, 16);
+                    s += __shfl_xor(s, 2, 16); q += __shfl_xor(q, 2, 16);
+                    s += __shfl_xor(s, 1, 16); q += __shfl_xor(q, 1, 16);
+                    if (rl == 0) {
+                        int cl = w * 32 + nt * 16 + quad * 4 + r;
+                        atomicAdd(&csum[cl], s);
+                        atomicAdd(&csq[cl], q);
+                    }
+                }
+            __syncthreads();
+            if (tid < 128) {
+                atomicAdd(bn + 256 + tid, csum[tid]);
+                atomicAdd(bn + 384 + tid, csq[tid]);
+            }
+            __syncthreads();
+        }
+    }
+    grid.sync();
+
     if (tid < 128) {
         float invN = 1.f / (float)N;
         float mu = bn[256 + tid] * invN;
@@ -602,16 +613,19 @@
         sB[tid] = bb2[tid] - mu * scl;
     }
     __syncthreads();
-    size_t idx = (size_t)blockIdx.x * 256 + tid;
-    size_t total = (size_t)N * 32;
-    if (idx < total) {
-        int c0 = (int)((idx * 4) & 127);
-        float4 v = *(const float4*)(out + idx * 4);
-        v.x = fmaf(v.x, sS[c0 + 0], sB[c0 + 0]);
-        v.y = fmaf(v.y, sS[c0 + 1], sB[c0 + 1]);
-        v.z = fmaf(v.z, sS[c0 + 2], sB[c0 + 2]);
-        v.w = fmaf(v.w, sS[c0 + 3], sB[c0 + 3]);
-        *(float4*)(out + idx * 4) = v;
+    const size_t total = (size_t)N * 32;
+    const int U9 = (int)((total + 255) / 256);
+    for (int u = blockIdx.x; u < U9; u += G) {
+        size_t idx = (size_t)u * 256 + tid;
+        if (idx < total) {
+            int c0 = (int)((idx * 4) & 127);
+            float4 v = *(const float4*)(out + idx * 4);
+            v.x = fmaf(v.x, sS[c0 + 0], sB[c0 + 0]);
+            v.y = fmaf(v.y, sS[c0 + 1], sB[c0 + 1]);
+            v.z = fmaf(v.z, sS[c0 + 2], sB[c0 + 2]);
+            v.w = fmaf(v.w, sS[c0 + 3], sB[c0 + 3]);
+            *(float4*)(out + idx * 4) = v;
+        }
     }
 }
 
@@ -639,9 +653,9 @@
 
     int N = in_sizes[0] / 128;
     int E = in_sizes[1];
-    const int slabs = (N + 127) / 128;
-    const int nsb = (N + 2047) / 2048;
-    const int nhb = (E + 255) / 256;
+    int slabs = (N + 127) / 128;
+    int nsb = (N + 2047) / 2048;
+    int nhb = (E + 255) / 256;
     const size_t B1 = (size_t)slabs * 32768;
 
     char* Wp = (char*)d_ws;
@@ -661,21 +675,43 @@
     float* sfold = (float*)(Wp + base + 263168);
     float* bfold = (float*)(Wp + base + 263680);
     float* bn    = (float*)(Wp + base + 264192);
-    int* ready   = (int*)(Wp + base + 266240);
+    int* bsum    = (int*)(Wp + base + 266240);
     int* cursor  = (int*)(Wp + base + 266496);
     int* rowptr  = (int*)(Wp + base + 266496 + (size_t)N * 4);
     int* csr     = (int*)(Wp + base + 266496 + (size_t)N * 8 + 8);
 
-    hipMemsetAsync(Wp + base + 264192, 0, 2304 + (size_t)N * 4, stream);
-    k_prep_hist<<<nhb + slabs * 2, 256, 0, stream>>>(
-        h, hb, WQ, WK, WV, WO, W2, Wqb, Wkb, Wvb, Wob, W2b, cursor, dst, N, E, nhb);
-    k_qkv_scan<<<nsb + slabs * 6, 256, 0, stream>>>(
-        hb, Wqb, Wkb, Wvb, Qb, KVb, cursor, rowptr, ready, N, nsb);
+    static int ncu = 0, nb1 = 0, nb2 = 0;
+    if (ncu == 0) {
+        int dev = 0;
+        hipGetDevice(&dev);
+        hipDeviceGetAttribute(&ncu, hipDeviceAttributeMultiprocessorCount, dev);
+        hipOccupancyMaxActiveBlocksPerMultiprocessor(&nb1, k_front, 256, 0);
+        hipOccupancyMaxActiveBlocksPerMultiprocessor(&nb2, k_back, 256, 0);
+        if (ncu <= 0) ncu = 256;
+        if (nb1 <= 0) nb1 = 1;
+        if (nb2 <= 0) nb2 = 1;
+    }
+    int G1 = ncu * nb1; if (G1 > 2048) G1 = 2048;
+    int G2 = ncu * nb2; if (G2 > 1024) G2 = 1024;
+    if (G1 < nsb) G1 = nsb;
+
+    {
+        void* a1[] = {(void*)&h, (void*)&hb, (void*)&WQ, (void*)&WK, (void*)&WV,
+                      (void*)&WO, (void*)&W2, (void*)&Wqb, (void*)&Wkb, (void*)&Wvb,
+                      (void*)&Wob, (void*)&W2b, (void*)&Qb, (void*)&KVb,
+                      (void*)&cursor, (void*)&rowptr, (void*)&bsum, (void*)&bn,
+                      (void*)&dst, (void*)&N, (void*)&E, (void*)&nhb, (void*)&nsb,
+                      (void*)&slabs};
+        hipLaunchCooperativeKernel((void*)k_front, dim3(G1), dim3(256), a1, 0, stream);
+    }
     k_scatter<<<nhb, 256, 0, stream>>>(src, dst, cursor, csr, E);
     k_attn<<<(N + 3) / 4, 256, 0, stream>>>(Qb, KVb, rowptr, csr, hb, N);
-    k_oproj<<<dim3(slabs, 2), 256, 0, stream>>>(hb, Wob, h, bO, t1b, bn, N);
-    k_fold1<<<256, 128, 0, stream>>>(bn, g1, bb1, W1, b1, W1b, badj, sfold, bfold, N);
-    k_ffn1<<<dim3(slabs, 2, 2), 256, 0, stream>>>(t1b, W1b, badj, ub, N);
-    k_ffn2<<<dim3(slabs, 2), 256, 0, stream>>>(ub, W2b, t1b, sfold, bfold, b2, out, bn, N);
-    k_bn2<<<(int)(((size_t)N * 32 + 255) / 256), 256, 0, stream>>>(out, bn, g2, bb2, N);
-}
+    {
+        void* a2[] = {(void*)&hb, (void*)&Wob, (void*)&h, (void*)&bO, (void*)&t1b,
+                      (void*)&bn, (void*)&g1, (void*)&bb1, (void*)&W1, (void*)&b1,
+                      (void*)&W1b, (void*)&badj, (void*)&sfold, (void*)&bfold,
+                      (void*)&ub, (void*)&W2b, (void*)&b2, (void*)&out,
+                      (void*)&g2, (void*)&bb2, (void*)&N, (void*)&slabs};
+        hipLaunchCooperativeKernel((void*)k_back, dim3(G2), dim3(256), a2, 0, stream);
+    }
+}
```

Result: slower. 666.2 us (+95.9%).
